# Optimization experiments

Measured on AMD Instinct MI355X. Metric: run time of the kernel, lower is better.

## Reference

```python
import jax, jax.numpy as jnp
import numpy as np

G = 64  # fixed grid size hardcoded in the torch module

def setup_inputs() -> dict:
    key = jax.random.key(0)
    ks = jax.random.split(key, 12)
    N, H = 500000, 256
    s = lambda fan_in: 1.0 / np.sqrt(fan_in)
    return {
        "positions": jax.random.normal(ks[0], (N, 3), jnp.float32) * 2.0,
        "grid_points": jax.random.normal(ks[1], (G, 3), jnp.float32) * 2.0,
        "W1": jax.random.normal(ks[2], (3, 64), jnp.float32) * s(3),
        "b1": jnp.zeros((64,), jnp.float32),
        "W2": jax.random.normal(ks[3], (64, 128), jnp.float32) * s(64),
        "b2": jnp.zeros((128,), jnp.float32),
        "W3": jax.random.normal(ks[4], (128, H), jnp.float32) * s(128),
        "b3": jnp.zeros((H,), jnp.float32),
        "Wn1": jax.random.normal(ks[5], (H, H), jnp.float32) * s(H),
        "bn1": jnp.zeros((H,), jnp.float32),
        "Wn2": jax.random.normal(ks[6], (H, H), jnp.float32) * s(H),
        "bn2": jnp.zeros((H,), jnp.float32),
        "Wh1": jax.random.normal(ks[7], (4, H, 128), jnp.float32) * s(H),
        "bh1": jnp.zeros((4, 128), jnp.float32),
        "Wh2": jax.random.normal(ks[8], (4, 128, 1), jnp.float32) * s(128),
        "bh2": jnp.zeros((4, 1), jnp.float32),
    }

def reference(positions, grid_points, W1, b1, W2, b2, W3, b3,
              Wn1, bn1, Wn2, bn2, Wh1, bh1, Wh2, bh2):
    # crystal_encoder: per-atom MLP 3 -> 64 -> 128 -> 256 over ALL N atoms
    h = jax.nn.relu(positions @ W1 + b1)
    h = jax.nn.relu(h @ W2 + b2)
    feat = h @ W3 + b3                                   # [N, H]

    # _map_crystal_to_grid: only the first min(N, 64) atoms are mapped.
    pos64 = positions[:G]                                # [64, 3]
    d2 = jnp.sum((pos64[:, None, :] - grid_points[None, :, :]) ** 2, axis=-1)
    idx = jnp.argmin(d2, axis=-1)                        # [64] nearest grid point per atom
    winner = jnp.full((G,), -1, jnp.int32).at[idx].max(jnp.arange(G, dtype=jnp.int32))
    grid_feats = jnp.where(winner[:, None] >= 0,
                           feat[jnp.clip(winner, 0)], 0.0)  # [64, H]

    # TetrahedralAGINetwork (per-node MLP, channels-first output convention)
    x = grid_feats[None]                                 # [1, 64, H]
    y = jax.nn.relu(x @ Wn1 + bn1) @ Wn2 + bn2           # [1, 64, H]
    agg = jnp.mean(jnp.swapaxes(y, 1, 2), axis=-1)       # mean over nodes -> [1, H]

    # 4 property heads, batched: [4, 1, 1] -> [4] (order: band_gap,
    # elastic_modulus, thermal_conductivity, dielectric_constant)
    h1 = jax.nn.relu(jnp.einsum('bc,kcd->kbd', agg, Wh1) + bh1[:, None, :])
    props = jnp.einsum('kbd,kdo->kbo', h1, Wh2) + bh2[:, None, :]
    return props.reshape(4)
```

## Files before the change

kernel.cpp:

```cpp
#include <hip/hip_runtime.h>


__device__ __forceinline__ void async_cp16(const float* g, float* l) {
    __builtin_amdgcn_global_load_lds(
        (const __attribute__((address_space(1))) void*)g,
        (__attribute__((address_space(3))) void*)l, 16, 0, 0);
}
__device__ __forceinline__ void stage_contig(const float* g, float* l, int nfloats, int tid) {
    const int lane = tid & 63, wv = tid >> 6;
    const int ninst = nfloats >> 8;
    for (int i = wv; i < ninst; i += 4)
        async_cp16(g + i*256 + lane*4, l + i*256);
}
__device__ __forceinline__ void stage_slice32(const float* g, float* l, int ld, int j0, int nrows, int tid) {
    const int lane = tid & 63, wv = tid >> 6;
    const int r = lane >> 3, c4 = (lane & 7) << 2;
    const int ninst = nrows >> 3;
    for (int i = wv; i < ninst; i += 4)
        async_cp16(g + (i*8 + r)*ld + j0 + c4, l + i*256);
}

#define A_SMEM_BYTES (32768*4)

__global__ __launch_bounds__(256) void a_gf(
    const float* __restrict__ positions, const float* __restrict__ grid_pts,
    const float* __restrict__ W1, const float* __restrict__ b1,
    const float* __restrict__ W2, const float* __restrict__ b2,
    const float* __restrict__ W3, const float* __restrict__ b3,
    float* __restrict__ gf_ws)
{
    extern __shared__ float w3s[];
    __shared__ float pos_s[192], grid_s[192], w1_s[192], b1_s[64];
    __shared__ int   idx_s[64], win_s[8];
    __shared__ __align__(16) float h1s[8*64];
    __shared__ __align__(16) float h2s[8*128];

    const int tid = threadIdx.x;
    const int bg  = blockIdx.x;

    stage_contig(W3, w3s, 32768, tid);
    if (tid < 192) { pos_s[tid] = positions[tid]; grid_s[tid] = grid_pts[tid]; w1_s[tid] = W1[tid]; }
    if (tid >= 192) b1_s[tid - 192] = b1[tid - 192];
    const float bb2 = b2[tid & 127];
    const float bb3 = b3[tid];
    __syncthreads();

    if (tid < 64) {
        const float px = pos_s[tid*3], py = pos_s[tid*3+1], pz = pos_s[tid*3+2];
        float best = 3.4e38f; int bi = 0;
        for (int g = 0; g < 64; ++g) {
            const float dx = px - grid_s[g*3];
            const float dy = py - grid_s[g*3+1];
            const float dz = pz - grid_s[g*3+2];
            const float d2 = dx*dx + dy*dy + dz*dz;
            if (d2 < best) { best = d2; bi = g; }
        }
        idx_s[tid] = bi;
    }
    __syncthreads();
    if (tid < 8) {
        const int g = bg*8 + tid;
        int m = -1;
        for (int i = 0; i < 64; ++i) if (idx_s[i] == g) m = i;
        win_s[tid] = m;
    }
    __syncthreads();

    #pragma unroll
    for (int u = 0; u < 2; ++u) {
        const int e  = tid + u*256;
        const int lr = e >> 6, k = e & 63;
        int r = win_s[lr]; if (r < 0) r = 0;
        const float acc = b1_s[k] + pos_s[r*3]*w1_s[k] + pos_s[r*3+1]*w1_s[64+k]
                                  + pos_s[r*3+2]*w1_s[128+k];
        h1s[lr*64 + k] = fmaxf(acc, 0.f);
    }
    __syncthreads();

    {
        const int d = tid & 127, t0 = tid >> 7;
        float acc[4];
        #pragma unroll
        for (int m = 0; m < 4; ++m) acc[m] = bb2;
        for (int kc = 0; kc < 64; kc += 16) {
            float w[16];
            #pragma unroll
            for (int u = 0; u < 16; ++u) w[u] = W2[(kc+u)*128 + d];
            #pragma unroll
            for (int u = 0; u < 16; u += 4) {
                #pragma unroll
                for (int m = 0; m < 4; ++m) {
                    const float4 h4 = *(const float4*)&h1s[(t0 + 2*m)*64 + kc + u];
                    acc[m] += h4.x*w[u] + h4.y*w[u+1] + h4.z*w[u+2] + h4.w*w[u+3];
                }
            }
        }
        #pragma unroll
        for (int m = 0; m < 4; ++m)
            h2s[(t0 + 2*m)*128 + d] = fmaxf(acc[m], 0.f);
    }
    __syncthreads();

    {
        const int j = tid;
        float ag[8];
        #pragma unroll
        for (int t = 0; t < 8; ++t) ag[t] = 0.f;
        for (int dc = 0; dc < 128; dc += 16) {
            float w[16];
            #pragma unroll
            for (int u = 0; u < 16; ++u) w[u] = w3s[(dc+u)*256 + j];
            #pragma unroll
            for (int u = 0; u < 16; u += 4) {
                #pragma unroll
                for (int t = 0; t < 8; ++t) {
                    const float4 h4 = *(const float4*)&h2s[t*128 + dc + u];
                    ag[t] += h4.x*w[u] + h4.y*w[u+1] + h4.z*w[u+2] + h4.w*w[u+3];
                }
            }
        }
        #pragma unroll
        for (int t = 0; t < 8; ++t)
            gf_ws[(bg*8 + t)*256 + j] = (win_s[t] >= 0) ? (ag[t] + bb3) : 0.f;
    }
}

__global__ __launch_bounds__(256) void k2_tpart(
    const float* __restrict__ Wn1, const float* __restrict__ bn1,
    const float* __restrict__ gf_ws, float* __restrict__ tpart_ws)
{
    __shared__ __align__(16) float wn1_s[256*32];
    __shared__ __align__(16) float gf_s[8*256];
    __shared__ float r_s[256];

    const int tid = threadIdx.x;
    const int bg  = blockIdx.x >> 3;
    const int j0  = (blockIdx.x & 7) * 32;
    stage_slice32(Wn1, wn1_s, 256, j0, 256, tid);
    stage_contig(gf_ws + bg*8*256, gf_s, 8*256, tid);

    const int jl = tid & 31, t = tid >> 5;
    const float bb = bn1[j0 + jl];
    __syncthreads();

    float acc = bb;
    for (int cc = 0; cc < 256; cc += 32) {
        float w[32];
        #pragma unroll
        for (int u = 0; u < 32; ++u) w[u] = wn1_s[(cc+u)*32 + jl];
        #pragma unroll
        for (int u = 0; u < 32; u += 4) {
            const float4 g4 = *(const float4*)&gf_s[t*256 + cc + u];
            acc += g4.x*w[u] + g4.y*w[u+1] + g4.z*w[u+2] + g4.w*w[u+3];
        }
    }
    r_s[tid] = fmaxf(acc, 0.f);
    __syncthreads();
    if (t == 0) {
        float ps = 0.f;
        #pragma unroll
        for (int tt = 0; tt < 8; ++tt) ps += r_s[tt*32 + jl];
        tpart_ws[bg*256 + j0 + jl] = ps;
    }
}

#define CD_SMEM_BYTES (32768*4)

__global__ __launch_bounds__(256) void cd_head(
    const float* __restrict__ Wn2, const float* __restrict__ bn2,
    const float* __restrict__ Wh1, const float* __restrict__ bh1,
    const float* __restrict__ Wh2, const float* __restrict__ bh2,
    const float* __restrict__ tpart_ws,
    float* __restrict__ out)
{
    extern __shared__ float sm[];
    __shared__ __align__(16) float tp_s[2048];
    __shared__ __align__(16) float tbar_s[256];
    __shared__ __align__(16) float agg_s[256];
    __shared__ __align__(16) float h1h_s[128];
    __shared__ __align__(16) float wh2_s[128];

    float* bufA = sm;
    float* bufB = sm + 16384;

    const int tid = threadIdx.x;
    const int k   = blockIdx.x;

    stage_contig(tpart_ws, tp_s, 2048, tid);
    stage_contig(Wn2,          bufA, 16384, tid);
    stage_contig(Wn2 + 16384,  bufB, 16384, tid);
    const float bbn2  = bn2[tid];
    const float bbh1k = (tid < 128) ? bh1[k*128 + tid] : 0.f;
    if (tid < 128) wh2_s[tid] = Wh2[k*128 + tid];
    const float bbh2k = bh2[k];
    __syncthreads();

    {
        float tb = 0.f;
        #pragma unroll
        for (int q = 0; q < 8; ++q) tb += tp_s[q*256 + tid];
        tbar_s[tid] = tb * (1.f/64.f);
    }
    __syncthreads();

    float acc = bbn2;
    for (int jc = 0; jc < 64; jc += 32) {
        float w[32];
        #pragma unroll
        for (int u = 0; u < 32; ++u) w[u] = bufA[(jc+u)*256 + tid];
        #pragma unroll
        for (int u = 0; u < 32; u += 4) {
            const float4 t4 = *(const float4*)&tbar_s[jc + u];
            acc += t4.x*w[u] + t4.y*w[u+1] + t4.z*w[u+2] + t4.w*w[u+3];
        }
    }
    __syncthreads();
    stage_contig(Wn2 + 32768, bufA, 16384, tid);
    for (int jc = 64; jc < 128; jc += 32) {
        float w[32];
        #pragma unroll
        for (int u = 0; u < 32; ++u) w[u] = bufB[(jc-64+u)*256 + tid];
        #pragma unroll
        for (int u = 0; u < 32; u += 4) {
            const float4 t4 = *(const float4*)&tbar_s[jc + u];
            acc += t4.x*w[u] + t4.y*w[u+1] + t4.z*w[u+2] + t4.w*w[u+3];
        }
    }
    __syncthreads();
    stage_contig(Wn2 + 49152, bufB, 16384, tid);
    for (int jc = 128; jc < 192; jc += 32) {
        float w[32];
        #pragma unroll
        for (int u = 0; u < 32; ++u) w[u] = bufA[(jc-128+u)*256 + tid];
        #pragma unroll
        for (int u = 0; u < 32; u += 4) {
            const float4 t4 = *(const float4*)&tbar_s[jc + u];
            acc += t4.x*w[u] + t4.y*w[u+1] + t4.z*w[u+2] + t4.w*w[u+3];
        }
    }
    __syncthreads();
    for (int jc = 192; jc < 256; jc += 32) {
        float w[32];
        #pragma unroll
        for (int u = 0; u < 32; ++u) w[u] = bufB[(jc-192+u)*256 + tid];
        #pragma unroll
        for (int u = 0; u < 32; u += 4) {
            const float4 t4 = *(const float4*)&tbar_s[jc + u];
            acc += t4.x*w[u] + t4.y*w[u+1] + t4.z*w[u+2] + t4.w*w[u+3];
        }
    }
    agg_s[tid] = acc;
    __syncthreads();
    stage_contig(Wh1 + k*32768,         bufA, 16384, tid);
    stage_contig(Wh1 + k*32768 + 16384, bufB, 16384, tid);
    __syncthreads();

    if (tid < 128) {
        const int d = tid;
        float a = bbh1k;
        for (int cc = 0; cc < 128; cc += 16) {
            float wa[16];
            #pragma unroll
            for (int u = 0; u < 16; ++u) wa[u] = bufA[(cc+u)*128 + d];
            #pragma unroll
            for (int u = 0; u < 16; u += 4) {
                const float4 a4 = *(const float4*)&agg_s[cc + u];
                a += a4.x*wa[u] + a4.y*wa[u+1] + a4.z*wa[u+2] + a4.w*wa[u+3];
            }
        }
        for (int cc = 128; cc < 256; cc += 16) {
            float wa[16];
            #pragma unroll
            for (int u = 0; u < 16; ++u) wa[u] = bufB[(cc-128+u)*128 + d];
            #pragma unroll
            for (int u = 0; u < 16; u += 4) {
                const float4 a4 = *(const float4*)&agg_s[cc + u];
                a += a4.x*wa[u] + a4.y*wa[u+1] + a4.z*wa[u+2] + a4.w*wa[u+3];
            }
        }
        h1h_s[d] = fmaxf(a, 0.f);
    }
    __syncthreads();
    if (tid == 0) {
        float a = bbh2k;
        for (int d = 0; d < 128; ++d) a += h1h_s[d] * wh2_s[d];
        out[k] = a;
    }
}

extern "C" void kernel_launch(void* const* d_in, const int* in_sizes, int n_in,
                              void* d_out, int out_size, void* d_ws, size_t ws_size,
                              hipStream_t stream) {
    const float* positions = (const float*)d_in[0];
    const float* grid      = (const float*)d_in[1];
    const float* W1  = (const float*)d_in[2];
    const float* b1  = (const float*)d_in[3];
    const float* W2  = (const float*)d_in[4];
    const float* b2  = (const float*)d_in[5];
    const float* W3  = (const float*)d_in[6];
    const float* b3  = (const float*)d_in[7];
    const float* Wn1 = (const float*)d_in[8];
    const float* bn1 = (const float*)d_in[9];
    const float* Wn2 = (const float*)d_in[10];
    const float* bn2 = (const float*)d_in[11];
    const float* Wh1 = (const float*)d_in[12];
    const float* bh1 = (const float*)d_in[13];
    const float* Wh2 = (const float*)d_in[14];
    const float* bh2 = (const float*)d_in[15];
    float* out = (float*)d_out;

    char* ws = (char*)d_ws;
    float* gf_ws    = (float*)(ws + 0);
    float* tpart_ws = (float*)(ws + 65536);

    (void)hipFuncSetAttribute((const void*)a_gf,
                              hipFuncAttributeMaxDynamicSharedMemorySize,
                              A_SMEM_BYTES);
    (void)hipFuncSetAttribute((const void*)cd_head,
                              hipFuncAttributeMaxDynamicSharedMemorySize,
                              CD_SMEM_BYTES);

    hipLaunchKernelGGL(a_gf,     dim3(8),  dim3(256), A_SMEM_BYTES, stream,
                       positions, grid, W1, b1, W2, b2, W3, b3, gf_ws);
    hipLaunchKernelGGL(k2_tpart, dim3(64), dim3(256), 0, stream,
                       Wn1, bn1, gf_ws, tpart_ws);
    hipLaunchKernelGGL(cd_head,  dim3(4),  dim3(256), CD_SMEM_BYTES, stream,
                       Wn2, bn2, Wh1, bh1, Wh2, bh2, tpart_ws, out);
}
```

Baseline: 110.1 us.

## Fuse grid-feature encoder and first node-MLP layer into one kernel

Merges the grid-feature kernel and the Wn1 partial-sum kernel into a single launch of 64 blocks. Each block recomputes the 8-atom encoder features in shared memory, then reuses the W3 shared buffer to stage its Wn1 column slice. This removes one kernel launch and the global workspace round trip for grid features. In exchange, the encoder work and W3 staging are repeated eight times per atom group.

```diff
diff --git a/kernel.cpp b/kernel.cpp
--- a/kernel.cpp
+++ b/kernel.cpp
@@ -20,29 +20,35 @@
         async_cp16(g + (i*8 + r)*ld + j0 + c4, l + i*256);
 }
 
-#define A_SMEM_BYTES (32768*4)
-
-__global__ __launch_bounds__(256) void a_gf(
+#define AB_SMEM_BYTES (32768*4)
+
+__global__ __launch_bounds__(256) void ab_tpart(
     const float* __restrict__ positions, const float* __restrict__ grid_pts,
     const float* __restrict__ W1, const float* __restrict__ b1,
     const float* __restrict__ W2, const float* __restrict__ b2,
     const float* __restrict__ W3, const float* __restrict__ b3,
-    float* __restrict__ gf_ws)
+    const float* __restrict__ Wn1, const float* __restrict__ bn1,
+    float* __restrict__ tpart_ws)
 {
     extern __shared__ float w3s[];
     __shared__ float pos_s[192], grid_s[192], w1_s[192], b1_s[64];
     __shared__ int   idx_s[64], win_s[8];
     __shared__ __align__(16) float h1s[8*64];
     __shared__ __align__(16) float h2s[8*128];
+    __shared__ __align__(16) float gfs[8*256];
+    __shared__ float r_s[256];
 
     const int tid = threadIdx.x;
-    const int bg  = blockIdx.x;
+    const int bg  = blockIdx.x >> 3;
+    const int j0  = (blockIdx.x & 7) * 32;
+    const int jl  = tid & 31, tt5 = tid >> 5;
 
     stage_contig(W3, w3s, 32768, tid);
     if (tid < 192) { pos_s[tid] = positions[tid]; grid_s[tid] = grid_pts[tid]; w1_s[tid] = W1[tid]; }
     if (tid >= 192) b1_s[tid - 192] = b1[tid - 192];
-    const float bb2 = b2[tid & 127];
-    const float bb3 = b3[tid];
+    const float bb2  = b2[tid & 127];
+    const float bb3  = b3[tid];
+    const float bbn1 = bn1[j0 + jl];
     __syncthreads();
 
     if (tid < 64) {
@@ -121,45 +127,31 @@
         }
         #pragma unroll
         for (int t = 0; t < 8; ++t)
-            gf_ws[(bg*8 + t)*256 + j] = (win_s[t] >= 0) ? (ag[t] + bb3) : 0.f;
-    }
-}
-
-__global__ __launch_bounds__(256) void k2_tpart(
-    const float* __restrict__ Wn1, const float* __restrict__ bn1,
-    const float* __restrict__ gf_ws, float* __restrict__ tpart_ws)
-{
-    __shared__ __align__(16) float wn1_s[256*32];
-    __shared__ __align__(16) float gf_s[8*256];
-    __shared__ float r_s[256];
-
-    const int tid = threadIdx.x;
-    const int bg  = blockIdx.x >> 3;
-    const int j0  = (blockIdx.x & 7) * 32;
-    stage_slice32(Wn1, wn1_s, 256, j0, 256, tid);
-    stage_contig(gf_ws + bg*8*256, gf_s, 8*256, tid);
-
-    const int jl = tid & 31, t = tid >> 5;
-    const float bb = bn1[j0 + jl];
-    __syncthreads();
-
-    float acc = bb;
-    for (int cc = 0; cc < 256; cc += 32) {
-        float w[32];
-        #pragma unroll
-        for (int u = 0; u < 32; ++u) w[u] = wn1_s[(cc+u)*32 + jl];
-        #pragma unroll
-        for (int u = 0; u < 32; u += 4) {
-            const float4 g4 = *(const float4*)&gf_s[t*256 + cc + u];
-            acc += g4.x*w[u] + g4.y*w[u+1] + g4.z*w[u+2] + g4.w*w[u+3];
-        }
-    }
-    r_s[tid] = fmaxf(acc, 0.f);
-    __syncthreads();
-    if (t == 0) {
+            gfs[t*256 + tid] = (win_s[t] >= 0) ? (ag[t] + bb3) : 0.f;
+    }
+    __syncthreads();
+    stage_slice32(Wn1, w3s, 256, j0, 256, tid);
+    __syncthreads();
+
+    {
+        float acc = bbn1;
+        for (int cc = 0; cc < 256; cc += 32) {
+            float w[32];
+            #pragma unroll
+            for (int u = 0; u < 32; ++u) w[u] = w3s[(cc+u)*32 + jl];
+            #pragma unroll
+            for (int u = 0; u < 32; u += 4) {
+                const float4 g4 = *(const float4*)&gfs[tt5*256 + cc + u];
+                acc += g4.x*w[u] + g4.y*w[u+1] + g4.z*w[u+2] + g4.w*w[u+3];
+            }
+        }
+        r_s[tid] = fmaxf(acc, 0.f);
+    }
+    __syncthreads();
+    if (tt5 == 0) {
         float ps = 0.f;
         #pragma unroll
-        for (int tt = 0; tt < 8; ++tt) ps += r_s[tt*32 + jl];
+        for (int t = 0; t < 8; ++t) ps += r_s[t*32 + jl];
         tpart_ws[bg*256 + j0 + jl] = ps;
     }
 }
@@ -309,21 +301,18 @@
     const float* bh2 = (const float*)d_in[15];
     float* out = (float*)d_out;
 
-    char* ws = (char*)d_ws;
-    float* gf_ws    = (float*)(ws + 0);
-    float* tpart_ws = (float*)(ws + 65536);
-
-    (void)hipFuncSetAttribute((const void*)a_gf,
+    float* tpart_ws = (float*)d_ws;
+
+    (void)hipFuncSetAttribute((const void*)ab_tpart,
                               hipFuncAttributeMaxDynamicSharedMemorySize,
-                              A_SMEM_BYTES);
+                              AB_SMEM_BYTES);
     (void)hipFuncSetAttribute((const void*)cd_head,
                               hipFuncAttributeMaxDynamicSharedMemorySize,
                               CD_SMEM_BYTES);
 
-    hipLaunchKernelGGL(a_gf,     dim3(8),  dim3(256), A_SMEM_BYTES, stream,
-                       positions, grid, W1, b1, W2, b2, W3, b3, gf_ws);
-    hipLaunchKernelGGL(k2_tpart, dim3(64), dim3(256), 0, stream,
-                       Wn1, bn1, gf_ws, tpart_ws);
+    hipLaunchKernelGGL(ab_tpart, dim3(64), dim3(256), AB_SMEM_BYTES, stream,
+                       positions, grid, W1, b1, W2, b2, W3, b3, Wn1, bn1,
+                       tpart_ws);
     hipLaunchKernelGGL(cd_head,  dim3(4),  dim3(256), CD_SMEM_BYTES, stream,
                        Wn2, bn2, Wh1, bh1, Wh2, bh2, tpart_ws, out);
 }
```

After: 110.3 us. No clear change (+0.1%).
